# Performance work log

Hardware: AMD Instinct MI355X
Metric: run time of the kernel (lower is better)

## Reference

```python
import jax, jax.numpy as jnp
import numpy as np

V, H, B, S, J, T, NOP = 30000, 512, 16, 256, 10, 8, 4
NEG = -1e9


def setup_inputs() -> dict:
    key = jax.random.key(0)
    ks = jax.random.split(key, 10)
    return {
        "x": jax.random.randint(ks[0], (B, S), 0, V),
        "encoder_output": jax.random.normal(ks[1], (B, S, H), jnp.float32),
        "encoder_hidden": jax.random.normal(ks[2], (B, H), jnp.float32),
        "max_len": T,
        "emb_W": jax.random.normal(ks[3], (V, H), jnp.float32) * 0.02,
        "slot_emb": jax.random.normal(ks[4], (J, H), jnp.float32) * 0.1,
        "W_ih": jax.random.normal(ks[5], (3 * H, H), jnp.float32) * 0.02,
        "W_hh": jax.random.normal(ks[6], (3 * H, H), jnp.float32) * 0.02,
        "b_ih": jnp.zeros((3 * H,), jnp.float32),
        "b_hh": jnp.zeros((3 * H,), jnp.float32),
        "w_gen_W": jax.random.normal(ks[7], (1, 3 * H), jnp.float32) * 0.02,
        "w_gen_b": jnp.zeros((1,), jnp.float32),
        "action_W": jax.random.normal(ks[8], (NOP, H), jnp.float32) * 0.02,
        "action_b": jnp.zeros((NOP,), jnp.float32),
    }


def gru_step(xin, h, W_ih, W_hh, b_ih, b_hh):
    # xin, h: (J, B, H). PyTorch GRU gate order: r, z, n.
    gi = xin @ W_ih.T + b_ih
    gh = h @ W_hh.T + b_hh
    ir, iz, inn = jnp.split(gi, 3, axis=-1)
    hr, hz, hn = jnp.split(gh, 3, axis=-1)
    r = jax.nn.sigmoid(ir + hr)
    z = jax.nn.sigmoid(iz + hz)
    n = jnp.tanh(inn + r * hn)
    return (1.0 - z) * n + z * h


def reference(x, encoder_output, encoder_hidden, max_len, emb_W, slot_emb,
              W_ih, W_hh, b_ih, b_hh, w_gen_W, w_gen_b, action_W, action_b):
    nJ, nH = slot_emb.shape
    nB, nS = x.shape
    nV = emb_W.shape[0]
    mask = (x == 0)  # (B, S) pad mask
    xJ = jnp.broadcast_to(x[None], (nJ, nB, nS))
    jidx = jnp.arange(nJ)[:, None, None]
    bidx = jnp.arange(nB)[None, :, None]

    w0 = jnp.broadcast_to(slot_emb[:, None, :], (nJ, nB, nH))  # slot query per slot
    h0 = jnp.broadcast_to(encoder_hidden[None], (nJ, nB, nH))

    def step(carry, _):
        w, h = carry
        h = gru_step(w, h, W_ih, W_hh, b_ih, b_hh)
        # attention over encoder states
        attn_e = jnp.einsum('bsh,jbh->jbs', encoder_output, h)
        attn_e = jnp.where(mask[None], NEG, attn_e)
        attn_hist = jax.nn.softmax(attn_e, axis=-1)          # (J,B,S)
        context = jnp.einsum('jbs,bsh->jbh', attn_hist, encoder_output)
        # vocab distribution
        attn_vocab = jax.nn.softmax(h @ emb_W.T, axis=-1)    # (J,B,V)
        # pointer-generator mix
        gen_in = jnp.concatenate([w, h, context], axis=-1)   # (J,B,3H)
        p_gen = jax.nn.sigmoid(gen_in @ w_gen_W.T + w_gen_b) # (J,B,1)
        p_ctx = jnp.zeros((nJ, nB, nV), attn_vocab.dtype).at[jidx, bidx, xJ].add(attn_hist)
        p_final = p_gen * attn_vocab + (1.0 - p_gen) * p_ctx # (J,B,V)
        w_idx = jnp.argmax(p_final, axis=-1)                 # greedy next token
        w_next = emb_W[w_idx]                                # (J,B,H)
        return (w_next, h), (p_final, context)

    (_, _), (p_all, ctx_all) = jax.lax.scan(step, (w0, h0), None, length=max_len)
    # gate head uses context from first decode step (k == 0)
    gates = ctx_all[0] @ action_W.T + action_b               # (J,B,n_op)
    all_gate = jnp.transpose(gates, (1, 0, 2))               # (B,J,n_op)
    all_point = jnp.transpose(p_all, (2, 1, 0, 3))           # (B,J,T,V)
    return all_gate, all_point
```

## Files before the change

### kernel.cpp

```cpp
#include <hip/hip_runtime.h>
#include <math.h>

#define V 30000
#define H 512
#define NB 16
#define NS 256
#define NJ 10
#define NT 8
#define NOPS 4
#define NR 160
#define EV 30720
#define NEGV -1e9f

typedef __attribute__((ext_vector_type(8))) short short8;
typedef __attribute__((ext_vector_type(4))) float f32x4;

__device__ inline float bf2f(unsigned short s) {
    union { unsigned int u; float f; } c; c.u = ((unsigned int)s) << 16;
    return c.f;
}
__device__ inline unsigned short f2bf(float f) {
    union { float f; unsigned int u; } c; c.f = f;
    unsigned int u = c.u;
    u += 0x7fffu + ((u >> 16) & 1u);
    return (unsigned short)(u >> 16);
}

__global__ void k_setup_emb(const float* __restrict__ emb, unsigned short* __restrict__ emb_bf, int n8) {
    int gid = blockIdx.x * 256 + threadIdx.x;
    if (gid >= n8) return;
    const float4* src = (const float4*)emb + (size_t)gid * 2;
    float4 a = src[0], b = src[1];
    short8 o;
    o[0] = (short)f2bf(a.x); o[1] = (short)f2bf(a.y); o[2] = (short)f2bf(a.z); o[3] = (short)f2bf(a.w);
    o[4] = (short)f2bf(b.x); o[5] = (short)f2bf(b.y); o[6] = (short)f2bf(b.z); o[7] = (short)f2bf(b.w);
    *(short8*)(emb_bf + (size_t)gid * 8) = o;
}

__global__ void k_setup_small(const float* __restrict__ Wih, const float* __restrict__ Whh,
    unsigned short* wih_hi, unsigned short* wih_lo, unsigned short* whh_hi, unsigned short* whh_lo,
    const float* __restrict__ slot, const float* __restrict__ ench,
    float* w_g, unsigned short* w_hi, unsigned short* w_lo,
    float* h_g, unsigned short* h_hi, unsigned short* h_lo)
{
    int gid = blockIdx.x * 256 + threadIdx.x;
    if (gid < 786432) {
        float v1 = Wih[gid];
        unsigned short hi = f2bf(v1);
        wih_hi[gid] = hi; wih_lo[gid] = f2bf(v1 - bf2f(hi));
        float v2 = Whh[gid];
        hi = f2bf(v2);
        whh_hi[gid] = hi; whh_lo[gid] = f2bf(v2 - bf2f(hi));
    } else {
        int i = gid - 786432;
        if (i < NR * H) {
            int jb = i >> 9, d = i & 511;
            int j = jb >> 4, b = jb & 15;
            float wv = slot[j * H + d];
            w_g[i] = wv;
            unsigned short hi = f2bf(wv);
            w_hi[i] = hi; w_lo[i] = f2bf(wv - bf2f(hi));
            float hv = ench[b * H + d];
            h_g[i] = hv;
            hi = f2bf(hv);
            h_hi[i] = hi; h_lo[i] = f2bf(hv - bf2f(hi));
        }
    }
}

#define GRU_APAD 520
__global__ __launch_bounds__(256) void k_gru_gemm(
    const unsigned short* __restrict__ w_hi, const unsigned short* __restrict__ w_lo,
    const unsigned short* __restrict__ h_hi, const unsigned short* __restrict__ h_lo,
    const unsigned short* __restrict__ wih_hi, const unsigned short* __restrict__ wih_lo,
    const unsigned short* __restrict__ whh_hi, const unsigned short* __restrict__ whh_lo,
    float* __restrict__ gi, float* __restrict__ gh)
{
    __shared__ unsigned short Ah[16 * GRU_APAD];
    __shared__ unsigned short Al[16 * GRU_APAD];
    int nch = blockIdx.x, mt = blockIdx.y, z = blockIdx.z;
    const unsigned short* Asrc_hi = z ? h_hi : w_hi;
    const unsigned short* Asrc_lo = z ? h_lo : w_lo;
    const unsigned short* Bhi = z ? whh_hi : wih_hi;
    const unsigned short* Blo = z ? whh_lo : wih_lo;
    float* outp = z ? gh : gi;
    int t = threadIdx.x;
    for (int i = t; i < 2048; i += 256) {
        int matl = i >> 10;
        int row = (i >> 6) & 15;
        int seg = i & 63;
        const unsigned short* src = (matl ? Asrc_lo : Asrc_hi) + (mt * 16 + row) * 512 + seg * 8;
        unsigned short* dst = (matl ? Al : Ah) + row * GRU_APAD + seg * 8;
        *(short8*)dst = *(const short8*)src;
    }
    __syncthreads();
    int wv = t >> 6, lane = t & 63;
    int col15 = lane & 15, quad = lane >> 4;
    f32x4 acc0 = {0.f, 0.f, 0.f, 0.f}, acc1 = {0.f, 0.f, 0.f, 0.f};
    int c0 = nch * 128 + wv * 32 + col15;
    int c1 = c0 + 16;
    const unsigned short* bhp0 = Bhi + c0 * 512 + quad * 8;
    const unsigned short* bhp1 = Bhi + c1 * 512 + quad * 8;
    const unsigned short* blp0 = Blo + c0 * 512 + quad * 8;
    const unsigned short* blp1 = Blo + c1 * 512 + quad * 8;
    const unsigned short* ahp = Ah + col15 * GRU_APAD + quad * 8;
    const unsigned short* alp = Al + col15 * GRU_APAD + quad * 8;
#pragma unroll
    for (int ks = 0; ks < 16; ks++) {
        int ko = ks * 32;
        short8 bh0 = *(const short8*)(bhp0 + ko);
        short8 bh1 = *(const short8*)(bhp1 + ko);
        short8 bl0 = *(const short8*)(blp0 + ko);
        short8 bl1 = *(const short8*)(blp1 + ko);
        short8 ah = *(const short8*)(ahp + ko);
        short8 al = *(const short8*)(alp + ko);
        acc0 = __builtin_amdgcn_mfma_f32_16x16x32_bf16(ah, bh0, acc0, 0, 0, 0);
        acc1 = __builtin_amdgcn_mfma_f32_16x16x32_bf16(ah, bh1, acc1, 0, 0, 0);
        acc0 = __builtin_amdgcn_mfma_f32_16x16x32_bf16(ah, bl0, acc0, 0, 0, 0);
        acc1 = __builtin_amdgcn_mfma_f32_16x16x32_bf16(ah, bl1, acc1, 0, 0, 0);
        acc0 = __builtin_amdgcn_mfma_f32_16x16x32_bf16(al, bh0, acc0, 0, 0, 0);
        acc1 = __builtin_amdgcn_mfma_f32_16x16x32_bf16(al, bh1, acc1, 0, 0, 0);
    }
#pragma unroll
    for (int r = 0; r < 4; r++) {
        int row = mt * 16 + quad * 4 + r;
        outp[row * 1536 + c0] = acc0[r];
        outp[row * 1536 + c1] = acc1[r];
    }
}

__global__ __launch_bounds__(256) void k_attention(
    const float* __restrict__ gi, const float* __restrict__ gh,
    const float* __restrict__ b_ih, const float* __restrict__ b_hh,
    float* __restrict__ h_g, unsigned short* __restrict__ h_hi, unsigned short* __restrict__ h_lo,
    const float* __restrict__ enc, const int* __restrict__ x,
    const float* __restrict__ w_g, const float* __restrict__ wgenW, const float* __restrict__ wgenb,
    float* __restrict__ attn_g, float* __restrict__ pgen_g,
    float* __restrict__ ctx0, int store_ctx)
{
    __shared__ float h_lds[512];
    __shared__ float sc[256];
    __shared__ float red[256];
    int jb = blockIdx.x;
    int b = jb & 15;
    int t = threadIdx.x;
    for (int d = t; d < 512; d += 256) {
        int base = jb * 1536;
        float ir = gi[base + d]        + b_ih[d];
        float iz = gi[base + 512 + d]  + b_ih[512 + d];
        float in = gi[base + 1024 + d] + b_ih[1024 + d];
        float hr = gh[base + d]        + b_hh[d];
        float hz = gh[base + 512 + d]  + b_hh[512 + d];
        float hn = gh[base + 1024 + d] + b_hh[1024 + d];
        float hold = h_g[jb * 512 + d];
        float r = 1.f / (1.f + expf(-(ir + hr)));
        float z = 1.f / (1.f + expf(-(iz + hz)));
        float n = tanhf(in + r * hn);
        float hnew = (1.f - z) * n + z * hold;
        h_lds[d] = hnew;
        h_g[jb * 512 + d] = hnew;
        unsigned short hi = f2bf(hnew);
        h_hi[jb * 512 + d] = hi;
        h_lo[jb * 512 + d] = f2bf(hnew - bf2f(hi));
    }
    __syncthreads();
    int wid = t >> 6, lane = t & 63;
    float hreg[8];
#pragma unroll
    for (int i = 0; i < 8; i++) hreg[i] = h_lds[lane * 8 + i];
    const float* encb = enc + (size_t)b * NS * H;
    for (int s = wid; s < NS; s += 4) {
        const float4* er = (const float4*)(encb + s * 512 + lane * 8);
        float4 e0 = er[0], e1 = er[1];
        float p = e0.x * hreg[0] + e0.y * hreg[1] + e0.z * hreg[2] + e0.w * hreg[3]
                + e1.x * hreg[4] + e1.y * hreg[5] + e1.z * hreg[6] + e1.w * hreg[7];
#pragma unroll
        for (int off = 32; off > 0; off >>= 1) p += __shfl_down(p, off);
        if (lane == 0) sc[s] = (x[b * NS + s] == 0) ? NEGV : p;
    }
    __syncthreads();
    red[t] = sc[t];
    __syncthreads();
    for (int sft = 128; sft > 0; sft >>= 1) { if (t < sft) red[t] = fmaxf(red[t], red[t + sft]); __syncthreads(); }
    float m = red[0];
    __syncthreads();
    float e = expf(sc[t] - m);
    red[t] = e;
    __syncthreads();
    for (int sft = 128; sft > 0; sft >>= 1) { if (t < sft) red[t] += red[t + sft]; __syncthreads(); }
    float inv = 1.f / red[0];
    float p_s = e * inv;
    sc[t] = p_s;
    attn_g[jb * NS + t] = p_s;
    __syncthreads();
    float c0 = 0.f, c1 = 0.f;
    const float2* enc2 = (const float2*)encb + t;
    for (int s = 0; s < NS; s++) {
        float ps = sc[s];
        float2 ev = enc2[s * 256];
        c0 += ps * ev.x; c1 += ps * ev.y;
    }
    if (store_ctx) ((float2*)ctx0)[jb * 256 + t] = make_float2(c0, c1);
    int d0 = 2 * t, d1 = 2 * t + 1;
    float pg = wgenW[d0] * w_g[jb * 512 + d0] + wgenW[d1] * w_g[jb * 512 + d1]
             + wgenW[512 + d0] * h_lds[d0] + wgenW[512 + d1] * h_lds[d1]
             + wgenW[1024 + d0] * c0 + wgenW[1024 + d1] * c1;
    red[t] = pg;
    __syncthreads();
    for (int sft = 128; sft > 0; sft >>= 1) { if (t < sft) red[t] += red[t + sft]; __syncthreads(); }
    if (t == 0) pgen_g[jb] = 1.f / (1.f + expf(-(red[0] + wgenb[0])));
}

__global__ __launch_bounds__(256) void k_gates(const float* __restrict__ ctx0,
    const float* __restrict__ aW, const float* __restrict__ ab, float* __restrict__ out)
{
    __shared__ float red[256];
    int jb = blockIdx.x; int j = jb >> 4, b = jb & 15; int t = threadIdx.x;
    float part[4] = {0.f, 0.f, 0.f, 0.f};
    for (int d = t; d < 512; d += 256) {
        float c = ctx0[jb * 512 + d];
#pragma unroll
        for (int o = 0; o < 4; o++) part[o] += c * aW[o * 512 + d];
    }
    for (int o = 0; o < 4; o++) {
        red[t] = part[o];
        __syncthreads();
        for (int sft = 128; sft > 0; sft >>= 1) { if (t < sft) red[t] += red[t + sft]; __syncthreads(); }
        if (t == 0) out[(b * NJ + j) * NOPS + o] = red[0] + ab[o];
        __syncthreads();
    }
}

#define VPAD 136
__global__ __launch_bounds__(256) void k_vgemm(
    const unsigned short* __restrict__ h_hi, const unsigned short* __restrict__ emb_bf,
    unsigned short* __restrict__ E)
{
    __shared__ unsigned short A[160 * VPAD];
    int blk = blockIdx.x;
    int t = threadIdx.x;
    int wv = t >> 6, lane = t & 63, col15 = lane & 15, quad = lane >> 4;
    int v = blk * 128 + wv * 32 + col15;
    f32x4 acc[10][2];
#pragma unroll
    for (int m = 0; m < 10; m++) {
        acc[m][0] = (f32x4){0.f, 0.f, 0.f, 0.f};
        acc[m][1] = (f32x4){0.f, 0.f, 0.f, 0.f};
    }
    int v0c = min(v, V - 1);
    int v1c = min(v + 16, V - 1);
    for (int kc = 0; kc < 4; kc++) {
        __syncthreads();
        for (int i = t; i < 2560; i += 256) {
            int row = i >> 4, seg = i & 15;
            *(short8*)(A + row * VPAD + seg * 8) = *(const short8*)(h_hi + row * 512 + kc * 128 + seg * 8);
        }
        __syncthreads();
#pragma unroll
        for (int ks = 0; ks < 4; ks++) {
            int kl = ks * 32 + quad * 8;
            int kg = kc * 128 + kl;
            short8 b0 = *(const short8*)(emb_bf + (size_t)v0c * 512 + kg);
            short8 b1 = *(const short8*)(emb_bf + (size_t)v1c * 512 + kg);
#pragma unroll
            for (int m = 0; m < 10; m++) {
                short8 a = *(const short8*)(A + (m * 16 + col15) * VPAD + kl);
                acc[m][0] = __builtin_amdgcn_mfma_f32_16x16x32_bf16(a, b0, acc[m][0], 0, 0, 0);
                acc[m][1] = __builtin_amdgcn_mfma_f32_16x16x32_bf16(a, b1, acc[m][1], 0, 0, 0);
            }
        }
    }
#pragma unroll
    for (int m = 0; m < 10; m++) {
#pragma unroll
        for (int tile = 0; tile < 2; tile++) {
            int vv = v + tile * 16;
#pragma unroll
            for (int r = 0; r < 4; r++) {
                int row = m * 16 + quad * 4 + r;
                float val = acc[m][tile][r];
                unsigned short evs = (vv < V) ? f2bf(expf(val)) : (unsigned short)0;
                E[(size_t)row * EV + vv] = evs;
            }
        }
    }
}

__global__ __launch_bounds__(256) void k_finalize(
    const unsigned short* __restrict__ E, const float* __restrict__ pgen_g,
    const float* __restrict__ attn_g, const int* __restrict__ x,
    const float* __restrict__ emb, float* __restrict__ out,
    float* __restrict__ w_g, unsigned short* __restrict__ w_hi, unsigned short* __restrict__ w_lo,
    int tstep)
{
    __shared__ float red[256];
    __shared__ float bvs[256];
    __shared__ int bis[256];
    int jb = blockIdx.x, t = threadIdx.x;
    int j = jb >> 4, b = jb & 15;
    const unsigned short* Er = E + (size_t)jb * EV;
    float lsum = 0.f;
    for (int i = 0; i < 15; i++) {
        short8 ev = *(const short8*)(Er + (i * 256 + t) * 8);
#pragma unroll
        for (int k = 0; k < 8; k++) lsum += bf2f((unsigned short)ev[k]);
    }
    red[t] = lsum;
    __syncthreads();
    for (int sft = 128; sft > 0; sft >>= 1) { if (t < sft) red[t] += red[t + sft]; __syncthreads(); }
    float inv = 1.f / red[0];
    float pgen = pgen_g[jb];
    size_t outbase = (size_t)640 + ((size_t)(b * NJ + j) * NT + tstep) * V;
    float* op = out + outbase;
    float best = -1.f; int besti = 0x7fffffff;
    for (int i = 0; i < 15; i++) {
        int vb = (i * 256 + t) * 8;
        short8 ev = *(const short8*)(Er + vb);
#pragma unroll
        for (int k = 0; k < 8; k++) {
            int vv = vb + k;
            if (vv < V) {
                float p = pgen * bf2f((unsigned short)ev[k]) * inv;
                op[vv] = p;
                if (p > best || (p == best && vv < besti)) { best = p; besti = vv; }
            }
        }
    }
    __syncthreads();
    {
        int vv = x[b * NS + t];
        float a = (1.f - pgen) * attn_g[jb * NS + t];
        float old = atomicAdd(&op[vv], a);
        float cand = old + a;
        if (cand > best || (cand == best && vv < besti)) { best = cand; besti = vv; }
    }
    bvs[t] = best; bis[t] = besti;
    __syncthreads();
    for (int sft = 128; sft > 0; sft >>= 1) {
        if (t < sft) {
            if (bvs[t + sft] > bvs[t] || (bvs[t + sft] == bvs[t] && bis[t + sft] < bis[t])) {
                bvs[t] = bvs[t + sft]; bis[t] = bis[t + sft];
            }
        }
        __syncthreads();
    }
    int widx = bis[0];
    for (int d = t; d < 512; d += 256) {
        float val = emb[(size_t)widx * 512 + d];
        w_g[jb * 512 + d] = val;
        unsigned short hi = f2bf(val);
        w_hi[jb * 512 + d] = hi;
        w_lo[jb * 512 + d] = f2bf(val - bf2f(hi));
    }
}

extern "C" void kernel_launch(void* const* d_in, const int* in_sizes, int n_in,
                              void* d_out, int out_size, void* d_ws, size_t ws_size,
                              hipStream_t stream) {
    const int*   x     = (const int*)d_in[0];
    const float* enc   = (const float*)d_in[1];
    const float* ench  = (const float*)d_in[2];
    const float* embW  = (const float*)d_in[4];
    const float* slot  = (const float*)d_in[5];
    const float* Wih   = (const float*)d_in[6];
    const float* Whh   = (const float*)d_in[7];
    const float* bih   = (const float*)d_in[8];
    const float* bhh   = (const float*)d_in[9];
    const float* wgenW = (const float*)d_in[10];
    const float* wgenb = (const float*)d_in[11];
    const float* aW    = (const float*)d_in[12];
    const float* ab    = (const float*)d_in[13];
    float* out = (float*)d_out;

    char* ws = (char*)d_ws;
    size_t off = 0;
    auto carve = [&](size_t bytes) { char* p = ws + off; off += (bytes + 255) & ~(size_t)255; return p; };
    unsigned short* emb_bf = (unsigned short*)carve((size_t)V * H * 2);
    unsigned short* wih_hi = (unsigned short*)carve(786432 * 2);
    unsigned short* wih_lo = (unsigned short*)carve(786432 * 2);
    unsigned short* whh_hi = (unsigned short*)carve(786432 * 2);
    unsigned short* whh_lo = (unsigned short*)carve(786432 * 2);
    float* w_f32 = (float*)carve(NR * H * 4);
    float* h_f32 = (float*)carve(NR * H * 4);
    float* ctx0  = (float*)carve(NR * H * 4);
    unsigned short* w_hi = (unsigned short*)carve(NR * H * 2);
    unsigned short* w_lo = (unsigned short*)carve(NR * H * 2);
    unsigned short* h_hi = (unsigned short*)carve(NR * H * 2);
    unsigned short* h_lo = (unsigned short*)carve(NR * H * 2);
    float* gi   = (float*)carve(NR * 1536 * 4);
    float* gh   = (float*)carve(NR * 1536 * 4);
    float* attn = (float*)carve(NR * NS * 4);
    float* pgen = (float*)carve(NR * 4);
    unsigned short* E = (unsigned short*)carve((size_t)NR * EV * 2);

    k_setup_emb<<<7500, 256, 0, stream>>>(embW, emb_bf, (V * H) / 8);
    k_setup_small<<<3392, 256, 0, stream>>>(Wih, Whh, wih_hi, wih_lo, whh_hi, whh_lo,
                                            slot, ench, w_f32, w_hi, w_lo, h_f32, h_hi, h_lo);
    for (int t = 0; t < NT; t++) {
        k_gru_gemm<<<dim3(12, 10, 2), 256, 0, stream>>>(w_hi, w_lo, h_hi, h_lo,
                                                        wih_hi, wih_lo, whh_hi, whh_lo, gi, gh);
        k_attention<<<NR, 256, 0, stream>>>(gi, gh, bih, bhh, h_f32, h_hi, h_lo, enc, x,
                                            w_f32, wgenW, wgenb, attn, pgen, ctx0, t == 0 ? 1 : 0);
        if (t == 0) k_gates<<<NR, 256, 0, stream>>>(ctx0, aW, ab, out);
        k_vgemm<<<240, 256, 0, stream>>>(h_hi, emb_bf, E);
        k_finalize<<<NR, 256, 0, stream>>>(E, pgen, attn, x, embW, out, w_f32, w_hi, w_lo, t);
    }
}
```

Measured before the change: 1.239 ms.

## Fuse vocab softmax sum and argmax into vgemm epilogue, vectorize finalize

The vocab GEMM epilogue now stages exp values in shared memory, computes per-row partial sums and a packed (value,index) argmax per block, and combines them across blocks with atomics. It also writes E to global as coalesced short8 stores. Finalize no longer rescans E for the sum and argmax; it streams scaled probabilities with float4 stores and merges the dense argmax with the scatter-updated entries. The context reduction in attention is split across waves using float4 loads, and the gates kernel is folded into finalize to save a launch. The scatter-merge argmax assumes scattered positions only increase, so any dense position the pointer scatter did not touch is compared using the pre-scatter maximum.

```diff
diff --git a/kernel.cpp b/kernel.cpp
--- a/kernel.cpp
+++ b/kernel.cpp
@@ -13,6 +13,7 @@
 #define NEGV -1e9f
 
 typedef __attribute__((ext_vector_type(8))) short short8;
+typedef __attribute__((ext_vector_type(4))) short short4v;
 typedef __attribute__((ext_vector_type(4))) float f32x4;
 
 __device__ inline float bf2f(unsigned short s) {
@@ -24,6 +25,10 @@
     unsigned int u = c.u;
     u += 0x7fffu + ((u >> 16) & 1u);
     return (unsigned short)(u >> 16);
+}
+__device__ inline unsigned long long packkey(float f, int v) {
+    union { float f; unsigned int u; } c; c.f = f;
+    return ((unsigned long long)c.u << 32) | (unsigned int)(0x7FFFFFFF - v);
 }
 
 __global__ void k_setup_emb(const float* __restrict__ emb, unsigned short* __restrict__ emb_bf, int n8) {
@@ -136,14 +141,17 @@
     const float* __restrict__ enc, const int* __restrict__ x,
     const float* __restrict__ w_g, const float* __restrict__ wgenW, const float* __restrict__ wgenb,
     float* __restrict__ attn_g, float* __restrict__ pgen_g,
-    float* __restrict__ ctx0, int store_ctx)
+    float* __restrict__ ctx0, int store_ctx,
+    float* __restrict__ rowsum, unsigned long long* __restrict__ argpk)
 {
     __shared__ float h_lds[512];
     __shared__ float sc[256];
     __shared__ float red[256];
+    __shared__ float ctxp[4 * 512];
     int jb = blockIdx.x;
     int b = jb & 15;
     int t = threadIdx.x;
+    if (t == 0) { rowsum[jb] = 0.f; argpk[jb] = 0ull; }
     for (int d = t; d < 512; d += 256) {
         int base = jb * 1536;
         float ir = gi[base + d]        + b_ih[d];
@@ -193,48 +201,40 @@
     sc[t] = p_s;
     attn_g[jb * NS + t] = p_s;
     __syncthreads();
-    float c0 = 0.f, c1 = 0.f;
-    const float2* enc2 = (const float2*)encb + t;
-    for (int s = 0; s < NS; s++) {
-        float ps = sc[s];
-        float2 ev = enc2[s * 256];
-        c0 += ps * ev.x; c1 += ps * ev.y;
-    }
+    {
+        float cp[8] = {0.f,0.f,0.f,0.f,0.f,0.f,0.f,0.f};
+        const float* encw = encb + lane * 8;
+        for (int s = wid * 64; s < wid * 64 + 64; s++) {
+            float ps = sc[s];
+            const float4* er = (const float4*)(encw + s * 512);
+            float4 e0 = er[0], e1 = er[1];
+            cp[0] += ps * e0.x; cp[1] += ps * e0.y; cp[2] += ps * e0.z; cp[3] += ps * e0.w;
+            cp[4] += ps * e1.x; cp[5] += ps * e1.y; cp[6] += ps * e1.z; cp[7] += ps * e1.w;
+        }
+        float* cw = ctxp + wid * 512 + lane * 8;
+#pragma unroll
+        for (int i = 0; i < 8; i++) cw[i] = cp[i];
+    }
+    __syncthreads();
+    int d0 = 2 * t, d1 = 2 * t + 1;
+    float c0 = ctxp[d0] + ctxp[512 + d0] + ctxp[1024 + d0] + ctxp[1536 + d0];
+    float c1 = ctxp[d1] + ctxp[512 + d1] + ctxp[1024 + d1] + ctxp[1536 + d1];
     if (store_ctx) ((float2*)ctx0)[jb * 256 + t] = make_float2(c0, c1);
-    int d0 = 2 * t, d1 = 2 * t + 1;
     float pg = wgenW[d0] * w_g[jb * 512 + d0] + wgenW[d1] * w_g[jb * 512 + d1]
              + wgenW[512 + d0] * h_lds[d0] + wgenW[512 + d1] * h_lds[d1]
              + wgenW[1024 + d0] * c0 + wgenW[1024 + d1] * c1;
+    __syncthreads();
     red[t] = pg;
     __syncthreads();
     for (int sft = 128; sft > 0; sft >>= 1) { if (t < sft) red[t] += red[t + sft]; __syncthreads(); }
     if (t == 0) pgen_g[jb] = 1.f / (1.f + expf(-(red[0] + wgenb[0])));
-}
-
-__global__ __launch_bounds__(256) void k_gates(const float* __restrict__ ctx0,
-    const float* __restrict__ aW, const float* __restrict__ ab, float* __restrict__ out)
-{
-    __shared__ float red[256];
-    int jb = blockIdx.x; int j = jb >> 4, b = jb & 15; int t = threadIdx.x;
-    float part[4] = {0.f, 0.f, 0.f, 0.f};
-    for (int d = t; d < 512; d += 256) {
-        float c = ctx0[jb * 512 + d];
-#pragma unroll
-        for (int o = 0; o < 4; o++) part[o] += c * aW[o * 512 + d];
-    }
-    for (int o = 0; o < 4; o++) {
-        red[t] = part[o];
-        __syncthreads();
-        for (int sft = 128; sft > 0; sft >>= 1) { if (t < sft) red[t] += red[t + sft]; __syncthreads(); }
-        if (t == 0) out[(b * NJ + j) * NOPS + o] = red[0] + ab[o];
-        __syncthreads();
-    }
 }
 
 #define VPAD 136
 __global__ __launch_bounds__(256) void k_vgemm(
     const unsigned short* __restrict__ h_hi, const unsigned short* __restrict__ emb_bf,
-    unsigned short* __restrict__ E)
+    unsigned short* __restrict__ E, float* __restrict__ rowsum,
+    unsigned long long* __restrict__ argpk)
 {
     __shared__ unsigned short A[160 * VPAD];
     int blk = blockIdx.x;
@@ -270,69 +270,91 @@
             }
         }
     }
+    __syncthreads();
 #pragma unroll
     for (int m = 0; m < 10; m++) {
 #pragma unroll
         for (int tile = 0; tile < 2; tile++) {
             int vv = v + tile * 16;
+            int cl = wv * 32 + tile * 16 + col15;
 #pragma unroll
             for (int r = 0; r < 4; r++) {
                 int row = m * 16 + quad * 4 + r;
-                float val = acc[m][tile][r];
-                unsigned short evs = (vv < V) ? f2bf(expf(val)) : (unsigned short)0;
-                E[(size_t)row * EV + vv] = evs;
+                float ev = (vv < V) ? expf(acc[m][tile][r]) : 0.f;
+                A[row * VPAD + cl] = f2bf(ev);
             }
+        }
+    }
+    __syncthreads();
+    if (t < 160) {
+        float s = 0.f;
+        unsigned long long key = 0ull;
+#pragma unroll
+        for (int seg = 0; seg < 16; seg++) {
+            short8 ev = *(const short8*)(A + t * VPAD + seg * 8);
+#pragma unroll
+            for (int k = 0; k < 8; k++) {
+                float f = bf2f((unsigned short)ev[k]);
+                s += f;
+                unsigned long long kk = packkey(f, blk * 128 + seg * 8 + k);
+                key = (kk > key) ? kk : key;
+            }
+        }
+        atomicAdd(rowsum + t, s);
+        atomicMax(argpk + t, key);
+    }
+    {
+        int rsub = t >> 4, seg = t & 15;
+        for (int it = 0; it < 10; it++) {
+            int row = it * 16 + rsub;
+            short8 ev = *(const short8*)(A + row * VPAD + seg * 8);
+            *(short8*)(E + (size_t)row * EV + blk * 128 + seg * 8) = ev;
         }
     }
 }
 
 __global__ __launch_bounds__(256) void k_finalize(
     const unsigned short* __restrict__ E, const float* __restrict__ pgen_g,
+    const float* __restrict__ rowsum, const unsigned long long* __restrict__ argpk,
     const float* __restrict__ attn_g, const int* __restrict__ x,
     const float* __restrict__ emb, float* __restrict__ out,
     float* __restrict__ w_g, unsigned short* __restrict__ w_hi, unsigned short* __restrict__ w_lo,
+    const float* __restrict__ ctx0, const float* __restrict__ aW, const float* __restrict__ ab,
     int tstep)
 {
-    __shared__ float red[256];
     __shared__ float bvs[256];
     __shared__ int bis[256];
+    __shared__ float red[256];
     int jb = blockIdx.x, t = threadIdx.x;
     int j = jb >> 4, b = jb & 15;
+    float inv = 1.f / rowsum[jb];
+    float pgen = pgen_g[jb];
+    float scale = pgen * inv;
     const unsigned short* Er = E + (size_t)jb * EV;
-    float lsum = 0.f;
-    for (int i = 0; i < 15; i++) {
-        short8 ev = *(const short8*)(Er + (i * 256 + t) * 8);
-#pragma unroll
-        for (int k = 0; k < 8; k++) lsum += bf2f((unsigned short)ev[k]);
-    }
-    red[t] = lsum;
-    __syncthreads();
-    for (int sft = 128; sft > 0; sft >>= 1) { if (t < sft) red[t] += red[t + sft]; __syncthreads(); }
-    float inv = 1.f / red[0];
-    float pgen = pgen_g[jb];
     size_t outbase = (size_t)640 + ((size_t)(b * NJ + j) * NT + tstep) * V;
     float* op = out + outbase;
-    float best = -1.f; int besti = 0x7fffffff;
-    for (int i = 0; i < 15; i++) {
-        int vb = (i * 256 + t) * 8;
-        short8 ev = *(const short8*)(Er + vb);
-#pragma unroll
-        for (int k = 0; k < 8; k++) {
-            int vv = vb + k;
-            if (vv < V) {
-                float p = pgen * bf2f((unsigned short)ev[k]) * inv;
-                op[vv] = p;
-                if (p > best || (p == best && vv < besti)) { best = p; besti = vv; }
-            }
-        }
-    }
-    __syncthreads();
+    for (int c = 0; c < 29; c++) {
+        int vv = c * 1024 + t * 4;
+        short4v e = *(const short4v*)(Er + vv);
+        float4 p = make_float4(bf2f((unsigned short)e[0]) * scale, bf2f((unsigned short)e[1]) * scale,
+                               bf2f((unsigned short)e[2]) * scale, bf2f((unsigned short)e[3]) * scale);
+        *(float4*)(op + vv) = p;
+    }
+    if (t < 76) {
+        int vv = 29696 + t * 4;
+        short4v e = *(const short4v*)(Er + vv);
+        float4 p = make_float4(bf2f((unsigned short)e[0]) * scale, bf2f((unsigned short)e[1]) * scale,
+                               bf2f((unsigned short)e[2]) * scale, bf2f((unsigned short)e[3]) * scale);
+        *(float4*)(op + vv) = p;
+    }
+    __syncthreads();
+    float best; int besti;
     {
         int vv = x[b * NS + t];
         float a = (1.f - pgen) * attn_g[jb * NS + t];
         float old = atomicAdd(&op[vv], a);
-        float cand = old + a;
-        if (cand > best || (cand == best && vv < besti)) { best = cand; besti = vv; }
+        best = old + a;
+        besti = vv;
     }
     bvs[t] = best; bis[t] = besti;
     __syncthreads();
@@ -344,13 +366,36 @@
         }
         __syncthreads();
     }
-    int widx = bis[0];
+    int widx;
+    {
+        unsigned long long key = argpk[jb];
+        union { unsigned int u; float f; } c; c.u = (unsigned int)(key >> 32);
+        float db = c.f * scale;
+        int di = 0x7FFFFFFF - (int)(key & 0xFFFFFFFFu);
+        float sb = bvs[0]; int si = bis[0];
+        widx = (sb > db || (sb == db && si < di)) ? si : di;
+    }
     for (int d = t; d < 512; d += 256) {
         float val = emb[(size_t)widx * 512 + d];
         w_g[jb * 512 + d] = val;
         unsigned short hi = f2bf(val);
         w_hi[jb * 512 + d] = hi;
         w_lo[jb * 512 + d] = f2bf(val - bf2f(hi));
+    }
+    if (tstep == 0) {
+        float part[4] = {0.f, 0.f, 0.f, 0.f};
+        for (int d = t; d < 512; d += 256) {
+            float c = ctx0[jb * 512 + d];
+#pragma unroll
+            for (int o = 0; o < 4; o++) part[o] += c * aW[o * 512 + d];
+        }
+        for (int o = 0; o < 4; o++) {
+            __syncthreads();
+            red[t] = part[o];
+            __syncthreads();
+            for (int sft = 128; sft > 0; sft >>= 1) { if (t < sft) red[t] += red[t + sft]; __syncthreads(); }
+            if (t == 0) out[(b * NJ + j) * NOPS + o] = red[0] + ab[o];
+        }
     }
 }
 
@@ -391,6 +436,8 @@
     float* gh   = (float*)carve(NR * 1536 * 4);
     float* attn = (float*)carve(NR * NS * 4);
     float* pgen = (float*)carve(NR * 4);
+    float* rowsum = (float*)carve(NR * 4);
+    unsigned long long* argpk = (unsigned long long*)carve(NR * 8);
     unsigned short* E = (unsigned short*)carve((size_t)NR * EV * 2);
 
     k_setup_emb<<<7500, 256, 0, stream>>>(embW, emb_bf, (V * H) / 8);
@@ -400,9 +447,10 @@
         k_gru_gemm<<<dim3(12, 10, 2), 256, 0, stream>>>(w_hi, w_lo, h_hi, h_lo,
                                                         wih_hi, wih_lo, whh_hi, whh_lo, gi, gh);
         k_attention<<<NR, 256, 0, stream>>>(gi, gh, bih, bhh, h_f32, h_hi, h_lo, enc, x,
-                                            w_f32, wgenW, wgenb, attn, pgen, ctx0, t == 0 ? 1 : 0);
-        if (t == 0) k_gates<<<NR, 256, 0, stream>>>(ctx0, aW, ab, out);
-        k_vgemm<<<240, 256, 0, stream>>>(h_hi, emb_bf, E);
-        k_finalize<<<NR, 256, 0, stream>>>(E, pgen, attn, x, embW, out, w_f32, w_hi, w_lo, t);
-    }
-}
+                                            w_f32, wgenW, wgenb, attn, pgen, ctx0, t == 0 ? 1 : 0,
+                                            rowsum, argpk);
+        k_vgemm<<<240, 256, 0, stream>>>(h_hi, emb_bf, E, rowsum, argpk);
+        k_finalize<<<NR, 256, 0, stream>>>(E, pgen, rowsum, argpk, attn, x, embW, out,
+                                           w_f32, w_hi, w_lo, ctx0, aW, ab, t);
+    }
+}
```

Result: faster. 1.102 ms (-11.0%).
